# Kernel optimization log

Hardware: AMD Instinct MI355X
Metric: run time of the kernel (lower is better)

## Reference

```python
import jax, jax.numpy as jnp
import numpy as np

N, D, DOUT = 8192, 128, 128

def setup_inputs() -> dict:
    key = jax.random.key(0)
    k0, k1, k2, k3, k4 = jax.random.split(key, 5)
    return {
        "inputs": jnp.zeros((N, DOUT, 1, 2), jnp.float32),   # output buffer, scatter target
        "adj_pos": jax.random.uniform(k0, (N, N), jnp.float32),
        "adj_neg": jax.random.uniform(k1, (N, N), jnp.float32),
        "h0": jax.random.normal(k2, (N, D), jnp.float32),
        "WB0": jax.random.normal(k3, (DOUT, 2 * D), jnp.float32) * 0.05,
        "WU0": jax.random.normal(k4, (DOUT, 2 * D), jnp.float32) * 0.05,
        "start": 0,
        "end": N,
    }

def reference(inputs, adj_pos, adj_neg, h0, WB0, WU0, start, end):
    # self vectors for the row range [start, end)
    self_vec = h0[start:end]                                   # [n, D]

    def branch(adj, W):
        mask = adj[start:end]                                  # [n, N]
        # masked neighbor aggregation (dense adj matmul) + mean normalization
        agg = (mask @ h0) / jnp.sum(mask, axis=1, keepdims=True)  # [n, D]
        # concat(self-aggregate) -> small matmul (transpose_b=True) -> relu
        feat = jnp.concatenate([agg, self_vec], axis=1)        # [n, 2D]
        return jax.nn.relu(feat @ W.T)                         # [n, DOUT]

    # scatter-assign into the 4-D buffer, slot 0 = balanced, slot 1 = unbalanced
    inputs = inputs.at[start:end, :, 0, 0].set(branch(adj_pos, WB0))
    inputs = inputs.at[start:end, :, 0, 1].set(branch(adj_neg, WU0))
    return inputs
```

## Files before the change

### kernel.cpp

```cpp
#include <hip/hip_runtime.h>
#include <hip/hip_bf16.h>


typedef __bf16 bf16_t;
typedef __attribute__((ext_vector_type(4))) __bf16 bf16x4;
typedef __attribute__((ext_vector_type(8))) __bf16 bf16x8;
typedef __attribute__((ext_vector_type(4))) float f32x4;

#define KD    8192
#define DD    128
#define NROWS 8192
#define BK    32
#define NSTEP (KD / BK)
#define DEPTH 8
#define FLD   136

__device__ __forceinline__ bf16_t to_bf16(float x) { return (bf16_t)x; }

__device__ __forceinline__ bf16x8 cvt8(f32x4 a, f32x4 b) {
    bf16x8 r;
    r[0] = to_bf16(a[0]); r[1] = to_bf16(a[1]); r[2] = to_bf16(a[2]); r[3] = to_bf16(a[3]);
    r[4] = to_bf16(b[0]); r[5] = to_bf16(b[1]); r[6] = to_bf16(b[2]); r[7] = to_bf16(b[3]);
    return r;
}

__global__ void prep_h0T(const float* __restrict__ h0, bf16_t* __restrict__ h0T) {
    __shared__ bf16_t lt[128 * 72];
    const int tid = threadIdx.x;
    const int r0  = blockIdx.x * 64;
#pragma unroll
    for (int i = 0; i < 8; ++i) {
        const int e  = tid + i * 256;
        const int r  = e >> 5;
        const int c4 = e & 31;
        f32x4 v = *(const f32x4*)(h0 + (size_t)(r0 + r) * DD + c4 * 4);
        lt[(c4 * 4 + 0) * 72 + r] = to_bf16(v[0]);
        lt[(c4 * 4 + 1) * 72 + r] = to_bf16(v[1]);
        lt[(c4 * 4 + 2) * 72 + r] = to_bf16(v[2]);
        lt[(c4 * 4 + 3) * 72 + r] = to_bf16(v[3]);
    }
    __syncthreads();
    const int d = tid >> 1, half = tid & 1;
    const bf16_t* src = lt + d * 72 + half * 32;
#pragma unroll
    for (int j = 0; j < 4; ++j) {
        bf16x4 lo = *(const bf16x4*)(src + j * 4);
        bf16x4 hi = *(const bf16x4*)(src + 16 + j * 4);
        bf16x8 v;
        v[0] = lo[0]; v[1] = lo[1]; v[2] = lo[2]; v[3] = lo[3];
        v[4] = hi[0]; v[5] = hi[1]; v[6] = hi[2]; v[7] = hi[3];
        *(bf16x8*)(h0T + (size_t)d * KD + r0 + half * 32 + j * 8) = v;
    }
}

__global__ __launch_bounds__(256, 1)
void fused_gcn(const float* __restrict__ inputs0,
               const float* __restrict__ adj_pos,
               const float* __restrict__ adj_neg,
               const float* __restrict__ h0,
               const float* __restrict__ WB0,
               const float* __restrict__ WU0,
               const bf16_t* __restrict__ h0T,
               const int* __restrict__ startp,
               const int* __restrict__ endp,
               float* __restrict__ out) {
    __shared__ bf16_t feat[4][16 * FLD];

    const int tid  = threadIdx.x;
    const int wv   = tid >> 6;
    const int lane = tid & 63;
    const int l15  = lane & 15;
    const int quad = lane >> 4;
    const int br   = blockIdx.y;
    const int m0   = (blockIdx.x * 4 + wv) * 16;

    const float* __restrict__ adj  = br ? adj_neg : adj_pos;
    const float* __restrict__ Wmat = br ? WU0 : WB0;

    const float*  arow = adj + (size_t)(m0 + l15) * KD + quad * 4;
    const bf16_t* bp   = h0T + (size_t)l15 * KD + quad * 8;

    f32x4 acc[8];
#pragma unroll
    for (int j = 0; j < 8; ++j) acc[j] = (f32x4){0.f, 0.f, 0.f, 0.f};
    float rsum = 0.f;

    f32x4 a0[DEPTH], a1[DEPTH];
    bf16x8 bfr[2][8];
#pragma unroll
    for (int p = 0; p < DEPTH; ++p) {
        a0[p] = *(const f32x4*)(arow + p * BK);
        a1[p] = *(const f32x4*)(arow + p * BK + 16);
    }
#pragma unroll
    for (int p = 0; p < 2; ++p)
#pragma unroll
        for (int j = 0; j < 8; ++j)
            bfr[p][j] = *(const bf16x8*)(bp + (size_t)j * 16 * KD + p * BK);

    for (int kb = 0; kb < (NSTEP - DEPTH) / DEPTH; ++kb) {
#pragma unroll
        for (int i = 0; i < DEPTH; ++i) {
            const int kt = kb * DEPTH + i;
            f32x4 va = a0[i], vb = a1[i];
            rsum += va[0] + va[1] + va[2] + va[3] + vb[0] + vb[1] + vb[2] + vb[3];
            bf16x8 afrag = cvt8(va, vb);
            a0[i] = *(const f32x4*)(arow + (kt + DEPTH) * BK);
            a1[i] = *(const f32x4*)(arow + (kt + DEPTH) * BK + 16);
            __builtin_amdgcn_sched_barrier(0);
#pragma unroll
            for (int j = 0; j < 8; ++j)
                acc[j] = __builtin_amdgcn_mfma_f32_16x16x32_bf16(afrag, bfr[i & 1][j], acc[j], 0, 0, 0);
            __builtin_amdgcn_sched_barrier(0);
#pragma unroll
            for (int j = 0; j < 8; ++j)
                bfr[i & 1][j] = *(const bf16x8*)(bp + (size_t)j * 16 * KD + (kt + 2) * BK);
        }
    }

#pragma unroll
    for (int i = 0; i < DEPTH; ++i) {
        const int kt = NSTEP - DEPTH + i;
        f32x4 va = a0[i], vb = a1[i];
        rsum += va[0] + va[1] + va[2] + va[3] + vb[0] + vb[1] + vb[2] + vb[3];
        bf16x8 afrag = cvt8(va, vb);
#pragma unroll
        for (int j = 0; j < 8; ++j)
            acc[j] = __builtin_amdgcn_mfma_f32_16x16x32_bf16(afrag, bfr[i & 1][j], acc[j], 0, 0, 0);
        if (kt + 2 < NSTEP) {
#pragma unroll
            for (int j = 0; j < 8; ++j)
                bfr[i & 1][j] = *(const bf16x8*)(bp + (size_t)j * 16 * KD + (kt + 2) * BK);
        }
    }

    rsum += __shfl_xor(rsum, 16);
    rsum += __shfl_xor(rsum, 32);
    float inv_rs[4];
#pragma unroll
    for (int i = 0; i < 4; ++i)
        inv_rs[i] = 1.0f / __shfl(rsum, quad * 4 + i);

    bf16_t* fw = feat[wv];
#pragma unroll
    for (int j = 0; j < 8; ++j)
#pragma unroll
        for (int i = 0; i < 4; ++i)
            fw[(quad * 4 + i) * FLD + l15 + j * 16] = to_bf16(acc[j][i] * inv_rs[i]);

    __syncthreads();

    f32x4 o[8];
#pragma unroll
    for (int j = 0; j < 8; ++j) o[j] = (f32x4){0.f, 0.f, 0.f, 0.f};
#pragma unroll
    for (int ks = 0; ks < 8; ++ks) {
        bf16x8 af;
        if (ks < 4) {
            af = *(const bf16x8*)(fw + l15 * FLD + ks * 32 + quad * 8);
        } else {
            const float* hp = h0 + (size_t)(m0 + l15) * DD + (ks - 4) * 32 + quad * 8;
            af = cvt8(*(const f32x4*)(hp), *(const f32x4*)(hp + 4));
        }
#pragma unroll
        for (int j = 0; j < 8; ++j) {
            const float* wp = Wmat + (size_t)(j * 16 + l15) * 256 + ks * 32 + quad * 8;
            bf16x8 bf = cvt8(*(const f32x4*)(wp), *(const f32x4*)(wp + 4));
            o[j] = __builtin_amdgcn_mfma_f32_16x16x32_bf16(af, bf, o[j], 0, 0, 0);
        }
    }

    const int s = startp[0], e = endp[0];
#pragma unroll
    for (int j = 0; j < 8; ++j)
#pragma unroll
        for (int i = 0; i < 4; ++i) {
            const int grow = m0 + quad * 4 + i;
            const size_t idx = (size_t)grow * 256 + (size_t)(j * 16 + l15) * 2 + br;
            float v;
            if (grow >= s && grow < e) v = fmaxf(o[j][i], 0.f);
            else                       v = inputs0[idx];
            out[idx] = v;
        }
}

extern "C" void kernel_launch(void* const* d_in, const int* in_sizes, int n_in,
                              void* d_out, int out_size, void* d_ws, size_t ws_size,
                              hipStream_t stream) {
    const float* inputs0 = (const float*)d_in[0];
    const float* adj_pos = (const float*)d_in[1];
    const float* adj_neg = (const float*)d_in[2];
    const float* h0      = (const float*)d_in[3];
    const float* WB0     = (const float*)d_in[4];
    const float* WU0     = (const float*)d_in[5];
    const int*   startp  = (const int*)d_in[6];
    const int*   endp    = (const int*)d_in[7];
    float*       out     = (float*)d_out;

    const size_t need = (size_t)DD * KD * sizeof(bf16_t);
    bf16_t* h0T = (ws_size >= need) ? (bf16_t*)d_ws : (bf16_t*)d_in[0];

    prep_h0T<<<128, 256, 0, stream>>>(h0, h0T);
    dim3 grid(NROWS / 64, 2);
    fused_gcn<<<grid, 256, 0, stream>>>(inputs0, adj_pos, adj_neg, h0, WB0, WU0,
                                        h0T, startp, endp, out);
}
```

Measured before the change: 762.3 us.

## Split output columns across wave pairs and double the grid for occupancy

Each block now covers 32 rows instead of 64. Pairs of waves share the same 16 rows, and each wave computes one half of the 128 output columns. This halves the per-wave accumulators and B-fragment registers, lowers the prefetch depth, drops the sched_barriers, and raises launch_bounds to 2 blocks per CU. It also doubles the grid, aiming for more waves in flight to hide the memory latency of streaming the fp32 adjacency matrix. The cost is that each adjacency row is now loaded twice, once per wave in the pair, which doubles L2 traffic for the dominant operand unless the cache absorbs it.

After: 762.6 us. About the same (+0.0%).

```diff
diff --git a/kernel.cpp b/kernel.cpp
--- a/kernel.cpp
+++ b/kernel.cpp
@@ -12,7 +12,7 @@
 #define NROWS 8192
 #define BK    32
 #define NSTEP (KD / BK)
-#define DEPTH 8
+#define DEPTH 4
 #define FLD   136
 
 __device__ __forceinline__ bf16_t to_bf16(float x) { return (bf16_t)x; }
@@ -53,7 +53,7 @@
     }
 }
 
-__global__ __launch_bounds__(256, 1)
+__global__ __launch_bounds__(256, 2)
 void fused_gcn(const float* __restrict__ inputs0,
                const float* __restrict__ adj_pos,
                const float* __restrict__ adj_neg,
@@ -64,7 +64,7 @@
                const int* __restrict__ startp,
                const int* __restrict__ endp,
                float* __restrict__ out) {
-    __shared__ bf16_t feat[4][16 * FLD];
+    __shared__ bf16_t feat[2][16 * FLD];
 
     const int tid  = threadIdx.x;
     const int wv   = tid >> 6;
@@ -72,31 +72,31 @@
     const int l15  = lane & 15;
     const int quad = lane >> 4;
     const int br   = blockIdx.y;
-    const int m0   = (blockIdx.x * 4 + wv) * 16;
+    const int r    = wv >> 1;
+    const int h    = wv & 1;
+    const int m0   = blockIdx.x * 32 + r * 16;
 
     const float* __restrict__ adj  = br ? adj_neg : adj_pos;
     const float* __restrict__ Wmat = br ? WU0 : WB0;
 
     const float*  arow = adj + (size_t)(m0 + l15) * KD + quad * 4;
-    const bf16_t* bp   = h0T + (size_t)l15 * KD + quad * 8;
-
-    f32x4 acc[8];
-#pragma unroll
-    for (int j = 0; j < 8; ++j) acc[j] = (f32x4){0.f, 0.f, 0.f, 0.f};
+    const bf16_t* bp   = h0T + (size_t)(h * 64 + l15) * KD + quad * 8;
+
+    f32x4 acc[4];
+#pragma unroll
+    for (int j = 0; j < 4; ++j) acc[j] = (f32x4){0.f, 0.f, 0.f, 0.f};
     float rsum = 0.f;
 
     f32x4 a0[DEPTH], a1[DEPTH];
-    bf16x8 bfr[2][8];
+    bf16x8 bfr[DEPTH][4];
 #pragma unroll
     for (int p = 0; p < DEPTH; ++p) {
         a0[p] = *(const f32x4*)(arow + p * BK);
         a1[p] = *(const f32x4*)(arow + p * BK + 16);
-    }
-#pragma unroll
-    for (int p = 0; p < 2; ++p)
-#pragma unroll
-        for (int j = 0; j < 8; ++j)
+#pragma unroll
+        for (int j = 0; j < 4; ++j)
             bfr[p][j] = *(const bf16x8*)(bp + (size_t)j * 16 * KD + p * BK);
+    }
 
     for (int kb = 0; kb < (NSTEP - DEPTH) / DEPTH; ++kb) {
 #pragma unroll
@@ -105,33 +105,25 @@
             f32x4 va = a0[i], vb = a1[i];
             rsum += va[0] + va[1] + va[2] + va[3] + vb[0] + vb[1] + vb[2] + vb[3];
             bf16x8 afrag = cvt8(va, vb);
+#pragma unroll
+            for (int j = 0; j < 4; ++j)
+                acc[j] = __builtin_amdgcn_mfma_f32_16x16x32_bf16(afrag, bfr[i][j], acc[j], 0, 0, 0);
             a0[i] = *(const f32x4*)(arow + (kt + DEPTH) * BK);
             a1[i] = *(const f32x4*)(arow + (kt + DEPTH) * BK + 16);
-            __builtin_amdgcn_sched_barrier(0);
-#pragma unroll
-            for (int j = 0; j < 8; ++j)
-                acc[j] = __builtin_amdgcn_mfma_f32_16x16x32_bf16(afrag, bfr[i & 1][j], acc[j], 0, 0, 0);
-            __builtin_amdgcn_sched_barrier(0);
-#pragma unroll
-            for (int j = 0; j < 8; ++j)
-                bfr[i & 1][j] = *(const bf16x8*)(bp + (size_t)j * 16 * KD + (kt + 2) * BK);
+#pragma unroll
+            for (int j = 0; j < 4; ++j)
+                bfr[i][j] = *(const bf16x8*)(bp + (size_t)j * 16 * KD + (kt + DEPTH) * BK);
         }
     }
 
 #pragma unroll
     for (int i = 0; i < DEPTH; ++i) {
-        const int kt = NSTEP - DEPTH + i;
         f32x4 va = a0[i], vb = a1[i];
         rsum += va[0] + va[1] + va[2] + va[3] + vb[0] + vb[1] + vb[2] + vb[3];
         bf16x8 afrag = cvt8(va, vb);
 #pragma unroll
-        for (int j = 0; j < 8; ++j)
-            acc[j] = __builtin_amdgcn_mfma_f32_16x16x32_bf16(afrag, bfr[i & 1][j], acc[j], 0, 0, 0);
-        if (kt + 2 < NSTEP) {
-#pragma unroll
-            for (int j = 0; j < 8; ++j)
-                bfr[i & 1][j] = *(const bf16x8*)(bp + (size_t)j * 16 * KD + (kt + 2) * BK);
-        }
+        for (int j = 0; j < 4; ++j)
+            acc[j] = __builtin_amdgcn_mfma_f32_16x16x32_bf16(afrag, bfr[i][j], acc[j], 0, 0, 0);
     }
 
     rsum += __shfl_xor(rsum, 16);
@@ -141,18 +133,18 @@
     for (int i = 0; i < 4; ++i)
         inv_rs[i] = 1.0f / __shfl(rsum, quad * 4 + i);
 
-    bf16_t* fw = feat[wv];
-#pragma unroll
-    for (int j = 0; j < 8; ++j)
+    bf16_t* fw = feat[r];
+#pragma unroll
+    for (int j = 0; j < 4; ++j)
 #pragma unroll
         for (int i = 0; i < 4; ++i)
-            fw[(quad * 4 + i) * FLD + l15 + j * 16] = to_bf16(acc[j][i] * inv_rs[i]);
+            fw[(quad * 4 + i) * FLD + h * 64 + j * 16 + l15] = to_bf16(acc[j][i] * inv_rs[i]);
 
     __syncthreads();
 
-    f32x4 o[8];
-#pragma unroll
-    for (int j = 0; j < 8; ++j) o[j] = (f32x4){0.f, 0.f, 0.f, 0.f};
+    f32x4 o[4];
+#pragma unroll
+    for (int j = 0; j < 4; ++j) o[j] = (f32x4){0.f, 0.f, 0.f, 0.f};
 #pragma unroll
     for (int ks = 0; ks < 8; ++ks) {
         bf16x8 af;
@@ -163,8 +155,8 @@
             af = cvt8(*(const f32x4*)(hp), *(const f32x4*)(hp + 4));
         }
 #pragma unroll
-        for (int j = 0; j < 8; ++j) {
-            const float* wp = Wmat + (size_t)(j * 16 + l15) * 256 + ks * 32 + quad * 8;
+        for (int j = 0; j < 4; ++j) {
+            const float* wp = Wmat + (size_t)(h * 64 + j * 16 + l15) * 256 + ks * 32 + quad * 8;
             bf16x8 bf = cvt8(*(const f32x4*)(wp), *(const f32x4*)(wp + 4));
             o[j] = __builtin_amdgcn_mfma_f32_16x16x32_bf16(af, bf, o[j], 0, 0, 0);
         }
@@ -172,11 +164,12 @@
 
     const int s = startp[0], e = endp[0];
 #pragma unroll
-    for (int j = 0; j < 8; ++j)
+    for (int j = 0; j < 4; ++j)
 #pragma unroll
         for (int i = 0; i < 4; ++i) {
             const int grow = m0 + quad * 4 + i;
-            const size_t idx = (size_t)grow * 256 + (size_t)(j * 16 + l15) * 2 + br;
+            const int col  = h * 64 + j * 16 + l15;
+            const size_t idx = (size_t)grow * 256 + (size_t)col * 2 + br;
             float v;
             if (grow >= s && grow < e) v = fmaxf(o[j][i], 0.f);
             else                       v = inputs0[idx];
@@ -201,7 +194,7 @@
     bf16_t* h0T = (ws_size >= need) ? (bf16_t*)d_ws : (bf16_t*)d_in[0];
 
     prep_h0T<<<128, 256, 0, stream>>>(h0, h0T);
-    dim3 grid(NROWS / 64, 2);
+    dim3 grid(NROWS / 32, 2);
     fused_gcn<<<grid, 256, 0, stream>>>(inputs0, adj_pos, adj_neg, h0, WB0, WU0,
                                         h0T, startp, endp, out);
 }
```

## Split K across waves with LDS reduction and two row-tiles per wave

Applied to the files above, without the earlier changes.

Each block now handles 32 rows, and each of its four waves takes a quarter of the K dimension for both 16-row tiles. The h0T fragments loaded once are therefore reused by two MFMA row groups. Partial accumulators and row sums are reduced through shared memory before normalisation and the small output matmul, which is now split across waves by row and column halves. Prefetch depth drops from 8 to 2 and launch bounds allow 2 blocks per CU. The goal is to halve h0T traffic per adjacency row and raise occupancy, at the cost of a large LDS reduction buffer and extra barriers.

New measurement: 636.2 us. 16.5% less time.

```diff
diff --git a/kernel.cpp b/kernel.cpp
--- a/kernel.cpp
+++ b/kernel.cpp
@@ -7,13 +7,14 @@
 typedef __attribute__((ext_vector_type(8))) __bf16 bf16x8;
 typedef __attribute__((ext_vector_type(4))) float f32x4;
 
-#define KD    8192
-#define DD    128
-#define NROWS 8192
-#define BK    32
-#define NSTEP (KD / BK)
-#define DEPTH 8
-#define FLD   136
+#define KD     8192
+#define DD     128
+#define NROWS  8192
+#define BK     32
+#define KQ     (KD / 4)
+#define NSTEPW (KQ / BK)
+#define DEPTH  2
+#define FLD    136
 
 __device__ __forceinline__ bf16_t to_bf16(float x) { return (bf16_t)x; }
 
@@ -53,7 +54,7 @@
     }
 }
 
-__global__ __launch_bounds__(256, 1)
+__global__ __launch_bounds__(256, 2)
 void fused_gcn(const float* __restrict__ inputs0,
                const float* __restrict__ adj_pos,
                const float* __restrict__ adj_neg,
@@ -64,7 +65,10 @@
                const int* __restrict__ startp,
                const int* __restrict__ endp,
                float* __restrict__ out) {
-    __shared__ bf16_t feat[4][16 * FLD];
+    __shared__ f32x4  accs[4 * 16 * 64];
+    __shared__ float  rsb[4][32];
+    __shared__ float  rst[32];
+    __shared__ bf16_t feat[32 * FLD];
 
     const int tid  = threadIdx.x;
     const int wv   = tid >> 6;
@@ -72,99 +76,142 @@
     const int l15  = lane & 15;
     const int quad = lane >> 4;
     const int br   = blockIdx.y;
-    const int m0   = (blockIdx.x * 4 + wv) * 16;
+    const int m0   = blockIdx.x * 32;
 
     const float* __restrict__ adj  = br ? adj_neg : adj_pos;
     const float* __restrict__ Wmat = br ? WU0 : WB0;
 
-    const float*  arow = adj + (size_t)(m0 + l15) * KD + quad * 4;
-    const bf16_t* bp   = h0T + (size_t)l15 * KD + quad * 8;
-
-    f32x4 acc[8];
-#pragma unroll
-    for (int j = 0; j < 8; ++j) acc[j] = (f32x4){0.f, 0.f, 0.f, 0.f};
-    float rsum = 0.f;
-
-    f32x4 a0[DEPTH], a1[DEPTH];
-    bf16x8 bfr[2][8];
+    const float*  arow0 = adj + (size_t)(m0 + l15) * KD + quad * 4 + wv * KQ;
+    const float*  arow1 = arow0 + (size_t)16 * KD;
+    const bf16_t* bp    = h0T + (size_t)l15 * KD + quad * 8 + wv * KQ;
+
+    f32x4 acc[2][8];
+#pragma unroll
+    for (int s = 0; s < 2; ++s)
+#pragma unroll
+        for (int j = 0; j < 8; ++j) acc[s][j] = (f32x4){0.f, 0.f, 0.f, 0.f};
+    float rs0 = 0.f, rs1 = 0.f;
+
+    f32x4 aA[DEPTH][2], aB[DEPTH][2];
+    bf16x8 bfr[DEPTH][8];
 #pragma unroll
     for (int p = 0; p < DEPTH; ++p) {
-        a0[p] = *(const f32x4*)(arow + p * BK);
-        a1[p] = *(const f32x4*)(arow + p * BK + 16);
-    }
-#pragma unroll
-    for (int p = 0; p < 2; ++p)
+        aA[p][0] = *(const f32x4*)(arow0 + p * BK);
+        aB[p][0] = *(const f32x4*)(arow0 + p * BK + 16);
+        aA[p][1] = *(const f32x4*)(arow1 + p * BK);
+        aB[p][1] = *(const f32x4*)(arow1 + p * BK + 16);
 #pragma unroll
         for (int j = 0; j < 8; ++j)
             bfr[p][j] = *(const bf16x8*)(bp + (size_t)j * 16 * KD + p * BK);
-
-    for (int kb = 0; kb < (NSTEP - DEPTH) / DEPTH; ++kb) {
+    }
+
+    for (int kb = 0; kb < (NSTEPW - DEPTH) / DEPTH; ++kb) {
 #pragma unroll
         for (int i = 0; i < DEPTH; ++i) {
             const int kt = kb * DEPTH + i;
-            f32x4 va = a0[i], vb = a1[i];
-            rsum += va[0] + va[1] + va[2] + va[3] + vb[0] + vb[1] + vb[2] + vb[3];
-            bf16x8 afrag = cvt8(va, vb);
-            a0[i] = *(const f32x4*)(arow + (kt + DEPTH) * BK);
-            a1[i] = *(const f32x4*)(arow + (kt + DEPTH) * BK + 16);
+            f32x4 va0 = aA[i][0], vb0 = aB[i][0];
+            f32x4 va1 = aA[i][1], vb1 = aB[i][1];
+            rs0 += va0[0] + va0[1] + va0[2] + va0[3] + vb0[0] + vb0[1] + vb0[2] + vb0[3];
+            rs1 += va1[0] + va1[1] + va1[2] + va1[3] + vb1[0] + vb1[1] + vb1[2] + vb1[3];
+            bf16x8 af0 = cvt8(va0, vb0);
+            bf16x8 af1 = cvt8(va1, vb1);
+            aA[i][0] = *(const f32x4*)(arow0 + (kt + DEPTH) * BK);
+            aB[i][0] = *(const f32x4*)(arow0 + (kt + DEPTH) * BK + 16);
+            aA[i][1] = *(const f32x4*)(arow1 + (kt + DEPTH) * BK);
+            aB[i][1] = *(const f32x4*)(arow1 + (kt + DEPTH) * BK + 16);
             __builtin_amdgcn_sched_barrier(0);
 #pragma unroll
             for (int j = 0; j < 8; ++j)
-                acc[j] = __builtin_amdgcn_mfma_f32_16x16x32_bf16(afrag, bfr[i & 1][j], acc[j], 0, 0, 0);
+                acc[0][j] = __builtin_amdgcn_mfma_f32_16x16x32_bf16(af0, bfr[i][j], acc[0][j], 0, 0, 0);
+#pragma unroll
+            for (int j = 0; j < 8; ++j)
+                acc[1][j] = __builtin_amdgcn_mfma_f32_16x16x32_bf16(af1, bfr[i][j], acc[1][j], 0, 0, 0);
             __builtin_amdgcn_sched_barrier(0);
 #pragma unroll
             for (int j = 0; j < 8; ++j)
-                bfr[i & 1][j] = *(const bf16x8*)(bp + (size_t)j * 16 * KD + (kt + 2) * BK);
+                bfr[i][j] = *(const bf16x8*)(bp + (size_t)j * 16 * KD + (kt + DEPTH) * BK);
         }
     }
 
 #pragma unroll
     for (int i = 0; i < DEPTH; ++i) {
-        const int kt = NSTEP - DEPTH + i;
-        f32x4 va = a0[i], vb = a1[i];
-        rsum += va[0] + va[1] + va[2] + va[3] + vb[0] + vb[1] + vb[2] + vb[3];
-        bf16x8 afrag = cvt8(va, vb);
-#pragma unroll
-        for (int j = 0; j < 8; ++j)
-            acc[j] = __builtin_amdgcn_mfma_f32_16x16x32_bf16(afrag, bfr[i & 1][j], acc[j], 0, 0, 0);
-        if (kt + 2 < NSTEP) {
-#pragma unroll
-            for (int j = 0; j < 8; ++j)
-                bfr[i & 1][j] = *(const bf16x8*)(bp + (size_t)j * 16 * KD + (kt + 2) * BK);
-        }
-    }
-
-    rsum += __shfl_xor(rsum, 16);
-    rsum += __shfl_xor(rsum, 32);
-    float inv_rs[4];
-#pragma unroll
-    for (int i = 0; i < 4; ++i)
-        inv_rs[i] = 1.0f / __shfl(rsum, quad * 4 + i);
-
-    bf16_t* fw = feat[wv];
-#pragma unroll
-    for (int j = 0; j < 8; ++j)
-#pragma unroll
-        for (int i = 0; i < 4; ++i)
-            fw[(quad * 4 + i) * FLD + l15 + j * 16] = to_bf16(acc[j][i] * inv_rs[i]);
-
-    __syncthreads();
-
-    f32x4 o[8];
-#pragma unroll
-    for (int j = 0; j < 8; ++j) o[j] = (f32x4){0.f, 0.f, 0.f, 0.f};
+        f32x4 va0 = aA[i][0], vb0 = aB[i][0];
+        f32x4 va1 = aA[i][1], vb1 = aB[i][1];
+        rs0 += va0[0] + va0[1] + va0[2] + va0[3] + vb0[0] + vb0[1] + vb0[2] + vb0[3];
+        rs1 += va1[0] + va1[1] + va1[2] + va1[3] + vb1[0] + vb1[1] + vb1[2] + vb1[3];
+        bf16x8 af0 = cvt8(va0, vb0);
+        bf16x8 af1 = cvt8(va1, vb1);
+#pragma unroll
+        for (int j = 0; j < 8; ++j)
+            acc[0][j] = __builtin_amdgcn_mfma_f32_16x16x32_bf16(af0, bfr[i][j], acc[0][j], 0, 0, 0);
+#pragma unroll
+        for (int j = 0; j < 8; ++j)
+            acc[1][j] = __builtin_amdgcn_mfma_f32_16x16x32_bf16(af1, bfr[i][j], acc[1][j], 0, 0, 0);
+    }
+
+    rs0 += __shfl_xor(rs0, 16);
+    rs0 += __shfl_xor(rs0, 32);
+    rs1 += __shfl_xor(rs1, 16);
+    rs1 += __shfl_xor(rs1, 32);
+    if (lane < 32) rsb[wv][lane] = (lane < 16) ? rs0 : rs1;
+
+#pragma unroll
+    for (int s = 0; s < 2; ++s)
+#pragma unroll
+        for (int j = 0; j < 8; ++j)
+            accs[((wv * 16 + s * 8 + j) << 6) + lane] = acc[s][j];
+
+    __syncthreads();
+
+    f32x4 red[2][2];
+#pragma unroll
+    for (int s = 0; s < 2; ++s)
+#pragma unroll
+        for (int jj = 0; jj < 2; ++jj) {
+            const int r4 = s * 8 + wv * 2 + jj;
+            f32x4 v = accs[((0 * 16 + r4) << 6) + lane];
+#pragma unroll
+            for (int ww = 1; ww < 4; ++ww)
+                v += accs[((ww * 16 + r4) << 6) + lane];
+            red[s][jj] = v;
+        }
+    if (wv == 0 && lane < 32) {
+        float t = rsb[0][lane] + rsb[1][lane] + rsb[2][lane] + rsb[3][lane];
+        rst[lane] = 1.0f / t;
+    }
+    __syncthreads();
+
+#pragma unroll
+    for (int s = 0; s < 2; ++s) {
+        float inv[4];
+#pragma unroll
+        for (int i = 0; i < 4; ++i) inv[i] = rst[s * 16 + quad * 4 + i];
+#pragma unroll
+        for (int jj = 0; jj < 2; ++jj)
+#pragma unroll
+            for (int i = 0; i < 4; ++i)
+                feat[(s * 16 + quad * 4 + i) * FLD + (wv * 2 + jj) * 16 + l15] =
+                    to_bf16(red[s][jj][i] * inv[i]);
+    }
+    __syncthreads();
+
+    const int s2 = wv >> 1;
+    const int h2 = wv & 1;
+    f32x4 o[4];
+#pragma unroll
+    for (int j = 0; j < 4; ++j) o[j] = (f32x4){0.f, 0.f, 0.f, 0.f};
 #pragma unroll
     for (int ks = 0; ks < 8; ++ks) {
         bf16x8 af;
         if (ks < 4) {
-            af = *(const bf16x8*)(fw + l15 * FLD + ks * 32 + quad * 8);
+            af = *(const bf16x8*)(feat + (s2 * 16 + l15) * FLD + ks * 32 + quad * 8);
         } else {
-            const float* hp = h0 + (size_t)(m0 + l15) * DD + (ks - 4) * 32 + quad * 8;
+            const float* hp = h0 + (size_t)(m0 + s2 * 16 + l15) * DD + (ks - 4) * 32 + quad * 8;
             af = cvt8(*(const f32x4*)(hp), *(const f32x4*)(hp + 4));
         }
 #pragma unroll
-        for (int j = 0; j < 8; ++j) {
-            const float* wp = Wmat + (size_t)(j * 16 + l15) * 256 + ks * 32 + quad * 8;
+        for (int j = 0; j < 4; ++j) {
+            const float* wp = Wmat + (size_t)(h2 * 64 + j * 16 + l15) * 256 + ks * 32 + quad * 8;
             bf16x8 bf = cvt8(*(const f32x4*)(wp), *(const f32x4*)(wp + 4));
             o[j] = __builtin_amdgcn_mfma_f32_16x16x32_bf16(af, bf, o[j], 0, 0, 0);
         }
@@ -172,11 +219,12 @@
 
     const int s = startp[0], e = endp[0];
 #pragma unroll
-    for (int j = 0; j < 8; ++j)
+    for (int j = 0; j < 4; ++j)
 #pragma unroll
         for (int i = 0; i < 4; ++i) {
-            const int grow = m0 + quad * 4 + i;
-            const size_t idx = (size_t)grow * 256 + (size_t)(j * 16 + l15) * 2 + br;
+            const int grow = m0 + s2 * 16 + quad * 4 + i;
+            const int col  = h2 * 64 + j * 16 + l15;
+            const size_t idx = (size_t)grow * 256 + (size_t)col * 2 + br;
             float v;
             if (grow >= s && grow < e) v = fmaxf(o[j][i], 0.f);
             else                       v = inputs0[idx];
@@ -201,7 +249,7 @@
     bf16_t* h0T = (ws_size >= need) ? (bf16_t*)d_ws : (bf16_t*)d_in[0];
 
     prep_h0T<<<128, 256, 0, stream>>>(h0, h0T);
-    dim3 grid(NROWS / 64, 2);
+    dim3 grid(NROWS / 32, 2);
     fused_gcn<<<grid, 256, 0, stream>>>(inputs0, adj_pos, adj_neg, h0, WB0, WU0,
                                         h0T, startp, endp, out);
 }
```
